# Kernel optimization log

Measured on AMD Instinct MI355X. Metric: run time of the kernel, lower is better.

The kernel has to match this reference:

```python
import jax, jax.numpy as jnp
import numpy as np

G = 16       # groups
GRID = 25    # hardcoded self.grid
EPS = 1e-5   # BatchNorm eps


def _gconv(x, w, pad):
    # x: (B, Cin, H, W), w: (Cout, Cin//G, kh, kw); grouped conv, stride 1
    return jax.lax.conv_general_dilated(
        x, w, window_strides=(1, 1), padding=[(pad, pad), (pad, pad)],
        feature_group_count=G)


def _bn_relu(h, g, b, m, v):
    # h: (G, B, C, H, W); per-group-instance BN params: (G, C). Inference BN.
    scale = (g / jnp.sqrt(v + EPS))[:, None, :, None, None]
    return jax.nn.relu((h - m[:, None, :, None, None]) * scale + b[:, None, :, None, None])


def setup_inputs() -> dict:
    key = jax.random.key(0)
    ks = jax.random.split(key, 11)
    B, C, H, W = 2, 256, 24, 24
    AC = GRID * C  # 6400 affinity channels
    return {
        "x":  jax.random.normal(ks[0], (B, C, H, W), jnp.float32),
        "W1": jax.random.normal(ks[1], (G, C, C // G, 3, 3), jnp.float32) * 0.05,
        "g1": jax.random.uniform(ks[2], (G, C), jnp.float32, 0.5, 1.5),
        "b1": jax.random.normal(ks[3], (G, C), jnp.float32) * 0.1,
        "m1": jax.random.normal(ks[4], (G, C), jnp.float32) * 0.1,
        "v1": jax.random.uniform(ks[5], (G, C), jnp.float32, 0.5, 1.5),
        "W2": jax.random.normal(ks[6], (G, AC, C // G, 1, 1), jnp.float32) * 0.05,
        "g2": jax.random.uniform(ks[7], (G, AC), jnp.float32, 0.5, 1.5),
        "b2": jax.random.normal(ks[8], (G, AC), jnp.float32) * 0.1,
        "m2": jax.random.normal(ks[9], (G, AC), jnp.float32) * 0.1,
        "v2": jax.random.uniform(ks[10], (G, AC), jnp.float32, 0.5, 1.5),
    }


def reference(x, W1, g1, b1, m1, v1, W2, g2, b2, m2, v2):
    B, C, H, W = x.shape
    Cg = C // G
    # 16 independent grouped 3x3 convs over the same input, batched via vmap
    h1 = jax.vmap(lambda w: _gconv(x, w, 1))(W1)          # (G, B, C, H, W)
    h1 = _bn_relu(h1, g1, b1, m1, v1)
    # grouped 1x1 conv with padding=1 (faithful to source -> spatial grows to H+2, W+2)
    a = jax.vmap(lambda h, w: _gconv(h, w, 1))(h1, W2)    # (G, B, 25C, H+2, W+2)
    a = _bn_relu(a, g2, b2, m2, v2)
    pooled = a.mean(axis=(-2, -1))                        # adaptive avg pool -> (G, B, 25C)
    xv = pooled.reshape(G, B, G, GRID * Cg)               # (G, B, G, 25*Cg)
    aff = jnp.einsum('ibkm,iblm->ibkl', xv, xv)           # (G, B, G, G) = theta @ phi
    idx = jnp.arange(G)
    aff_i = aff[idx, :, idx, :] / G                       # aff[:, i], /N  -> (G, B, G)
    ex = h1.reshape(G, B, G, Cg * H * W)
    # torch.matmul((B,G), (B,G,M)) broadcasts 2-D lhs -> (B, B, M); kept faithfully
    z = jnp.einsum('ipk,iqkm->ipqm', aff_i, ex)           # (G, B, B, Cg*H*W)
    z = z.reshape(G, B, B, Cg, H, W).transpose(1, 0, 2, 3, 4, 5)
    return z.reshape(B, G * B * Cg, H, W)                 # (B, B*C, H, W)
```

## Files before the change

kernel.cpp:

```cpp
#include <hip/hip_runtime.h>
#include <hip/hip_bf16.h>


typedef __attribute__((ext_vector_type(8))) short short8;
typedef __attribute__((ext_vector_type(4))) short short4v;
typedef __attribute__((ext_vector_type(4))) float f32x4;

static __device__ __forceinline__ short f2bf(float x) {
    unsigned u = __float_as_uint(x);
    unsigned r = (u + 0x7fffu + ((u >> 16) & 1u)) >> 16;
    return (short)r;
}

__global__ __launch_bounds__(256) void k1_conv_mfma(
    const float* __restrict__ xin,
    const float* __restrict__ W1,
    const float* __restrict__ g1, const float* __restrict__ b1,
    const float* __restrict__ m1, const float* __restrict__ v1,
    float* __restrict__ h1f)
{
    __shared__ __align__(16) short xs[27*26*24];
    __shared__ __align__(16) short wA[5*16*40];
    __shared__ float scale_s[16], bias_s[16];

    int bid = blockIdx.x;
    int i = bid >> 5, b = (bid >> 4) & 1, g = bid & 15;
    int t = threadIdx.x;

    int* xz = (int*)xs;
    for (int idx = t; idx < 27*26*12; idx += 256) xz[idx] = 0;
    if (t < 16) {
        int c = i*256 + g*16 + t;
        float sc = g1[c] * rsqrtf(v1[c] + 1e-5f);
        scale_s[t] = sc;
        bias_s[t]  = b1[c] - m1[c] * sc;
    }
    __syncthreads();

    const float* xb = &xin[(b*256 + g*16)*576];
    for (int idx = t; idx < 9216; idx += 256) {
        int ci = idx / 576; int s = idx - ci*576;
        int y = s / 24; int x = s - y*24;
        xs[((y+1)*26 + (x+1))*24 + ci] = f2bf(xb[idx]);
    }
    const float* wb = &W1[(i*256 + g*16)*144];
    for (int idx = t; idx < 2560; idx += 256) {
        int kk = idx >> 9, rem = idx & 511, co = rem >> 5, k = rem & 31;
        int tap = 2*kk + (k >> 4), ci = k & 15;
        float val = (tap < 9) ? wb[co*144 + ci*9 + tap] * scale_s[co] : 0.f;
        wA[(kk*16 + co)*40 + k] = f2bf(val);
    }
    __syncthreads();

    int l = t & 63, w = t >> 6;
    int quad = l >> 4, col = l & 15;
    int ci0 = (quad & 1) * 8;

    short8 afr[5];
#pragma unroll
    for (int kk = 0; kk < 5; kk++)
        afr[kk] = *(const short8*)&wA[(kk*16 + col)*40 + quad*8];

    f32x4 cb = *(const f32x4*)&bias_s[quad*4];

    const int offE[5] = {0, 48, 648, 1248, 1296};
    const int offO[5] = {24, 624, 672, 1272, 1872};
    int off[5];
#pragma unroll
    for (int kk = 0; kk < 5; kk++) off[kk] = (quad >= 2) ? offO[kk] : offE[kk];

    float* hout = &h1f[((i*2 + b)*256 + g*16)*576];
#pragma unroll 3
    for (int tt = 0; tt < 9; tt++) {
        int tile = w*9 + tt;
        int s = tile*16 + col;
        int y = s / 24; int x = s - y*24;
        int base = (y*26 + x)*24 + ci0;
        f32x4 acc = cb;
#pragma unroll
        for (int kk = 0; kk < 5; kk++) {
            short8 bf = *(const short8*)&xs[base + off[kk]];
            acc = __builtin_amdgcn_mfma_f32_16x16x32_bf16(afr[kk], bf, acc, 0, 0, 0);
        }
#pragma unroll
        for (int r = 0; r < 4; r++)
            hout[(quad*4 + r)*576 + s] = fmaxf(acc[r], 0.f);
    }
}

__global__ __launch_bounds__(256) void k2_pool_mfma(
    const float* __restrict__ h1f,
    const float* __restrict__ W2,
    const float* __restrict__ g2, const float* __restrict__ b2,
    const float* __restrict__ m2, const float* __restrict__ v2,
    float* __restrict__ pooled)
{
    __shared__ __align__(16) short hsb[576*20];
    __shared__ __align__(16) short wlb[400*16];
    __shared__ __align__(16) float psum[4*400];
    __shared__ __align__(16) float bias_s[400];

    int bid = blockIdx.x;
    int i = bid >> 5, b = (bid >> 4) & 1, k = bid & 15;
    int t = threadIdx.x;

    const float* hbase = &h1f[((i*2 + b)*256 + k*16)*576];
    for (int idx = t; idx < 9216; idx += 256) {
        int j = idx / 576; int s = idx - j*576;
        hsb[s*20 + j] = f2bf(hbase[idx]);
    }
    for (int m = t; m < 400; m += 256) {
        int o = i*6400 + k*400 + m;
        float s2 = g2[o] * rsqrtf(v2[o] + 1e-5f);
        bias_s[m] = b2[o] - m2[o] * s2;
        const float4* wr = (const float4*)&W2[o*16];
#pragma unroll
        for (int q = 0; q < 4; q++) {
            float4 wv = wr[q];
            wlb[m*16 + q*4 + 0] = f2bf(wv.x * s2);
            wlb[m*16 + q*4 + 1] = f2bf(wv.y * s2);
            wlb[m*16 + q*4 + 2] = f2bf(wv.z * s2);
            wlb[m*16 + q*4 + 3] = f2bf(wv.w * s2);
        }
    }
    __syncthreads();

    int l = t & 63, w = t >> 6;
    int half = l >> 4;
    int col  = l & 15;

    short8 bfr[9];
#pragma unroll
    for (int u = 0; u < 9; u++) {
        if (l < 32) {
            const short* p = &hsb[((w*9 + u)*16 + col)*20 + half*8];
            short4v lo = *(const short4v*)p;
            short4v hi = *(const short4v*)(p + 4);
            short8 f; f[0]=lo.x; f[1]=lo.y; f[2]=lo.z; f[3]=lo.w;
                      f[4]=hi.x; f[5]=hi.y; f[6]=hi.z; f[7]=hi.w;
            bfr[u] = f;
        } else {
            bfr[u] = (short8)0;
        }
    }

    for (int mt = 0; mt < 25; mt++) {
        short8 af = (short8)0;
        if (l < 32)
            af = *(const short8*)&wlb[(mt*16 + col)*16 + half*8];

        f32x4 cb = *(const f32x4*)&bias_s[mt*16 + half*4];

        f32x4 d[9];
#pragma unroll
        for (int u = 0; u < 9; u++)
            d[u] = __builtin_amdgcn_mfma_f32_16x16x32_bf16(af, bfr[u], cb, 0, 0, 0);

        float p0=0.f, p1=0.f, p2=0.f, p3=0.f;
#pragma unroll
        for (int u = 0; u < 9; u++) {
            p0 += fmaxf(d[u][0], 0.f);
            p1 += fmaxf(d[u][1], 0.f);
            p2 += fmaxf(d[u][2], 0.f);
            p3 += fmaxf(d[u][3], 0.f);
        }
#pragma unroll
        for (int msk = 1; msk < 16; msk <<= 1) {
            p0 += __shfl_xor(p0, msk);
            p1 += __shfl_xor(p1, msk);
            p2 += __shfl_xor(p2, msk);
            p3 += __shfl_xor(p3, msk);
        }
        if (col == 0) {
            f32x4 pv = {p0, p1, p2, p3};
            *(f32x4*)&psum[w*400 + mt*16 + half*4] = pv;
        }
    }
    __syncthreads();

    const float inv = 1.f / 676.f;
    for (int m = t; m < 400; m += 256) {
        float s = psum[0*400+m] + psum[1*400+m] + psum[2*400+m] + psum[3*400+m];
        float be = bias_s[m];
        pooled[(i*2+b)*6400 + k*400 + m] = (s + 100.f * fmaxf(be, 0.f)) * inv;
    }
}

__global__ __launch_bounds__(256) void k3_aff(const float* __restrict__ pooled,
                                              float* __restrict__ aff)
{
    __shared__ float th[400];
    __shared__ float parts[256];
    int bid = blockIdx.x;
    int i = bid >> 1;
    int t = threadIdx.x;
    const float* pb = &pooled[bid*6400];
    for (int idx = t; idx < 400; idx += 256) th[idx] = pb[i*400 + idx];
    __syncthreads();
    int l = t >> 4, p = t & 15;
    float sum = 0.f;
    const float* pl = &pb[l*400];
    for (int m = p*25; m < p*25 + 25; m++) sum = fmaf(th[m], pl[m], sum);
    parts[t] = sum;
    __syncthreads();
    if (t < 16) {
        float s = 0.f;
        for (int pp = 0; pp < 16; pp++) s += parts[t*16 + pp];
        aff[bid*16 + t] = s * (1.f/16.f);
    }
}

__global__ __launch_bounds__(256) void k4_out(const float* __restrict__ h1f,
                                              const float* __restrict__ aff,
                                              float* __restrict__ out)
{
    __shared__ float a0[16], a1[16];
    int bid = blockIdx.x;
    int i = bid >> 5, q = (bid >> 4) & 1, cg = bid & 15;
    int t = threadIdx.x;
    if (t < 16) a0[t] = aff[(i*2+0)*16 + t];
    else if (t < 32) a1[t-16] = aff[(i*2+1)*16 + (t-16)];
    __syncthreads();
    const float* hb = &h1f[((i*2+q)*256 + cg)*576];
    int ch = i*32 + q*16 + cg;
    for (int s = t; s < 576; s += 256) {
        float acc0 = 0.f, acc1 = 0.f;
#pragma unroll
        for (int k = 0; k < 16; k++) {
            float v = hb[k*9216 + s];
            acc0 = fmaf(a0[k], v, acc0);
            acc1 = fmaf(a1[k], v, acc1);
        }
        out[ch*576 + s]         = acc0;
        out[(512 + ch)*576 + s] = acc1;
    }
}

extern "C" void kernel_launch(void* const* d_in, const int* in_sizes, int n_in,
                              void* d_out, int out_size, void* d_ws, size_t ws_size,
                              hipStream_t stream)
{
    const float* x  = (const float*)d_in[0];
    const float* W1 = (const float*)d_in[1];
    const float* g1 = (const float*)d_in[2];
    const float* b1 = (const float*)d_in[3];
    const float* m1 = (const float*)d_in[4];
    const float* v1 = (const float*)d_in[5];
    const float* W2 = (const float*)d_in[6];
    const float* g2 = (const float*)d_in[7];
    const float* b2 = (const float*)d_in[8];
    const float* m2 = (const float*)d_in[9];
    const float* v2 = (const float*)d_in[10];

    float* h1f    = (float*)d_ws;
    float* pooled = h1f + 16*2*256*576;
    float* aff    = pooled + 16*2*6400;

    float* out = (float*)d_out;

    hipLaunchKernelGGL(k1_conv_mfma, dim3(512), dim3(256), 0, stream,
                       x, W1, g1, b1, m1, v1, h1f);
    hipLaunchKernelGGL(k2_pool_mfma, dim3(512), dim3(256), 0, stream,
                       h1f, W2, g2, b2, m2, v2, pooled);
    hipLaunchKernelGGL(k3_aff,       dim3(32),  dim3(256), 0, stream,
                       pooled, aff);
    hipLaunchKernelGGL(k4_out,       dim3(512), dim3(256), 0, stream,
                       h1f, aff, out);
}
```

Measured before the change: 126.5 us.

## Fuse grouped 3x3 conv and 1x1-conv pooling kernels via shared LDS

Merges the conv+BN+ReLU kernel and the 1x1 conv+BN+ReLU+pool kernel into one block-per-(i,b,g) kernel. The conv output stays in registers, is packed to bf16 straight into a reused LDS region, and feeds the second MFMA stage without a global round trip. h1f is still written to global because the final kernel reads it. This removes one launch and the global reread and conversion of h1f, at the cost of a larger fused kernel with more register pressure (9 accumulators held across a barrier).

Result: slower. 129.2 us (+2.1%).

```diff
diff --git a/kernel.cpp b/kernel.cpp
--- a/kernel.cpp
+++ b/kernel.cpp
@@ -12,16 +12,25 @@
     return (short)r;
 }
 
-__global__ __launch_bounds__(256) void k1_conv_mfma(
+__global__ __launch_bounds__(256) void k12_fused(
     const float* __restrict__ xin,
     const float* __restrict__ W1,
     const float* __restrict__ g1, const float* __restrict__ b1,
     const float* __restrict__ m1, const float* __restrict__ v1,
-    float* __restrict__ h1f)
-{
-    __shared__ __align__(16) short xs[27*26*24];
-    __shared__ __align__(16) short wA[5*16*40];
-    __shared__ float scale_s[16], bias_s[16];
+    const float* __restrict__ W2,
+    const float* __restrict__ g2, const float* __restrict__ b2,
+    const float* __restrict__ m2, const float* __restrict__ v2,
+    float* __restrict__ h1f,
+    float* __restrict__ pooled)
+{
+    __shared__ __align__(16) char smem[43840];
+    short* xs    = (short*)smem;
+    short* wA    = (short*)(smem + 33696);
+    short* hsb   = (short*)smem;
+    short* wlb   = (short*)(smem + 23040);
+    float* psum  = (float*)(smem + 35840);
+    float* bias2 = (float*)(smem + 42240);
+    __shared__ float scale1[16], bias1[16];
 
     int bid = blockIdx.x;
     int i = bid >> 5, b = (bid >> 4) & 1, g = bid & 15;
@@ -32,8 +41,8 @@
     if (t < 16) {
         int c = i*256 + g*16 + t;
         float sc = g1[c] * rsqrtf(v1[c] + 1e-5f);
-        scale_s[t] = sc;
-        bias_s[t]  = b1[c] - m1[c] * sc;
+        scale1[t] = sc;
+        bias1[t]  = b1[c] - m1[c] * sc;
     }
     __syncthreads();
 
@@ -47,72 +56,66 @@
     for (int idx = t; idx < 2560; idx += 256) {
         int kk = idx >> 9, rem = idx & 511, co = rem >> 5, k = rem & 31;
         int tap = 2*kk + (k >> 4), ci = k & 15;
-        float val = (tap < 9) ? wb[co*144 + ci*9 + tap] * scale_s[co] : 0.f;
+        float val = (tap < 9) ? wb[co*144 + ci*9 + tap] * scale1[co] : 0.f;
         wA[(kk*16 + co)*40 + k] = f2bf(val);
     }
     __syncthreads();
 
     int l = t & 63, w = t >> 6;
     int quad = l >> 4, col = l & 15;
-    int ci0 = (quad & 1) * 8;
-
-    short8 afr[5];
-#pragma unroll
-    for (int kk = 0; kk < 5; kk++)
-        afr[kk] = *(const short8*)&wA[(kk*16 + col)*40 + quad*8];
-
-    f32x4 cb = *(const f32x4*)&bias_s[quad*4];
-
-    const int offE[5] = {0, 48, 648, 1248, 1296};
-    const int offO[5] = {24, 624, 672, 1272, 1872};
-    int off[5];
-#pragma unroll
-    for (int kk = 0; kk < 5; kk++) off[kk] = (quad >= 2) ? offO[kk] : offE[kk];
-
-    float* hout = &h1f[((i*2 + b)*256 + g*16)*576];
+    {
+        int ci0 = (quad & 1) * 8;
+        short8 afr[5];
+#pragma unroll
+        for (int kk = 0; kk < 5; kk++)
+            afr[kk] = *(const short8*)&wA[(kk*16 + col)*40 + quad*8];
+        f32x4 cb1 = *(const f32x4*)&bias1[quad*4];
+
+        const int offE[5] = {0, 48, 648, 1248, 1296};
+        const int offO[5] = {24, 624, 672, 1272, 1872};
+        int off[5];
+#pragma unroll
+        for (int kk = 0; kk < 5; kk++) off[kk] = (quad >= 2) ? offO[kk] : offE[kk];
+
+        f32x4 dreg[9];
 #pragma unroll 3
-    for (int tt = 0; tt < 9; tt++) {
-        int tile = w*9 + tt;
-        int s = tile*16 + col;
-        int y = s / 24; int x = s - y*24;
-        int base = (y*26 + x)*24 + ci0;
-        f32x4 acc = cb;
-#pragma unroll
-        for (int kk = 0; kk < 5; kk++) {
-            short8 bf = *(const short8*)&xs[base + off[kk]];
-            acc = __builtin_amdgcn_mfma_f32_16x16x32_bf16(afr[kk], bf, acc, 0, 0, 0);
-        }
-#pragma unroll
-        for (int r = 0; r < 4; r++)
-            hout[(quad*4 + r)*576 + s] = fmaxf(acc[r], 0.f);
-    }
-}
-
-__global__ __launch_bounds__(256) void k2_pool_mfma(
-    const float* __restrict__ h1f,
-    const float* __restrict__ W2,
-    const float* __restrict__ g2, const float* __restrict__ b2,
-    const float* __restrict__ m2, const float* __restrict__ v2,
-    float* __restrict__ pooled)
-{
-    __shared__ __align__(16) short hsb[576*20];
-    __shared__ __align__(16) short wlb[400*16];
-    __shared__ __align__(16) float psum[4*400];
-    __shared__ __align__(16) float bias_s[400];
-
-    int bid = blockIdx.x;
-    int i = bid >> 5, b = (bid >> 4) & 1, k = bid & 15;
-    int t = threadIdx.x;
-
-    const float* hbase = &h1f[((i*2 + b)*256 + k*16)*576];
-    for (int idx = t; idx < 9216; idx += 256) {
-        int j = idx / 576; int s = idx - j*576;
-        hsb[s*20 + j] = f2bf(hbase[idx]);
-    }
+        for (int tt = 0; tt < 9; tt++) {
+            int s = (w*9 + tt)*16 + col;
+            int y = s / 24; int x = s - y*24;
+            int base = (y*26 + x)*24 + ci0;
+            f32x4 acc = cb1;
+#pragma unroll
+            for (int kk = 0; kk < 5; kk++) {
+                short8 bf = *(const short8*)&xs[base + off[kk]];
+                acc = __builtin_amdgcn_mfma_f32_16x16x32_bf16(afr[kk], bf, acc, 0, 0, 0);
+            }
+#pragma unroll
+            for (int r = 0; r < 4; r++) acc[r] = fmaxf(acc[r], 0.f);
+            dreg[tt] = acc;
+        }
+        __syncthreads();
+
+        float* hout = &h1f[((i*2 + b)*256 + g*16)*576];
+#pragma unroll
+        for (int tt = 0; tt < 9; tt++) {
+            int s = (w*9 + tt)*16 + col;
+            f32x4 acc = dreg[tt];
+            unsigned p0 = (unsigned)(unsigned short)f2bf(acc[0]) |
+                          ((unsigned)(unsigned short)f2bf(acc[1]) << 16);
+            unsigned p1 = (unsigned)(unsigned short)f2bf(acc[2]) |
+                          ((unsigned)(unsigned short)f2bf(acc[3]) << 16);
+            uint2 pk = {p0, p1};
+            *(uint2*)&hsb[s*20 + quad*4] = pk;
+#pragma unroll
+            for (int r = 0; r < 4; r++)
+                hout[(quad*4 + r)*576 + s] = acc[r];
+        }
+    }
+
     for (int m = t; m < 400; m += 256) {
-        int o = i*6400 + k*400 + m;
+        int o = i*6400 + g*400 + m;
         float s2 = g2[o] * rsqrtf(v2[o] + 1e-5f);
-        bias_s[m] = b2[o] - m2[o] * s2;
+        bias2[m] = b2[o] - m2[o] * s2;
         const float4* wr = (const float4*)&W2[o*16];
 #pragma unroll
         for (int q = 0; q < 4; q++) {
@@ -125,55 +128,54 @@
     }
     __syncthreads();
 
-    int l = t & 63, w = t >> 6;
     int half = l >> 4;
-    int col  = l & 15;
-
-    short8 bfr[9];
-#pragma unroll
-    for (int u = 0; u < 9; u++) {
-        if (l < 32) {
-            const short* p = &hsb[((w*9 + u)*16 + col)*20 + half*8];
-            short4v lo = *(const short4v*)p;
-            short4v hi = *(const short4v*)(p + 4);
-            short8 f; f[0]=lo.x; f[1]=lo.y; f[2]=lo.z; f[3]=lo.w;
-                      f[4]=hi.x; f[5]=hi.y; f[6]=hi.z; f[7]=hi.w;
-            bfr[u] = f;
-        } else {
-            bfr[u] = (short8)0;
-        }
-    }
-
-    for (int mt = 0; mt < 25; mt++) {
-        short8 af = (short8)0;
-        if (l < 32)
-            af = *(const short8*)&wlb[(mt*16 + col)*16 + half*8];
-
-        f32x4 cb = *(const f32x4*)&bias_s[mt*16 + half*4];
-
-        f32x4 d[9];
-#pragma unroll
-        for (int u = 0; u < 9; u++)
-            d[u] = __builtin_amdgcn_mfma_f32_16x16x32_bf16(af, bfr[u], cb, 0, 0, 0);
-
-        float p0=0.f, p1=0.f, p2=0.f, p3=0.f;
+    {
+        short8 bfr[9];
 #pragma unroll
         for (int u = 0; u < 9; u++) {
-            p0 += fmaxf(d[u][0], 0.f);
-            p1 += fmaxf(d[u][1], 0.f);
-            p2 += fmaxf(d[u][2], 0.f);
-            p3 += fmaxf(d[u][3], 0.f);
-        }
-#pragma unroll
-        for (int msk = 1; msk < 16; msk <<= 1) {
-            p0 += __shfl_xor(p0, msk);
-            p1 += __shfl_xor(p1, msk);
-            p2 += __shfl_xor(p2, msk);
-            p3 += __shfl_xor(p3, msk);
-        }
-        if (col == 0) {
-            f32x4 pv = {p0, p1, p2, p3};
-            *(f32x4*)&psum[w*400 + mt*16 + half*4] = pv;
+            if (l < 32) {
+                const short* p = &hsb[((w*9 + u)*16 + col)*20 + half*8];
+                short4v lo = *(const short4v*)p;
+                short4v hi = *(const short4v*)(p + 4);
+                short8 f; f[0]=lo.x; f[1]=lo.y; f[2]=lo.z; f[3]=lo.w;
+                          f[4]=hi.x; f[5]=hi.y; f[6]=hi.z; f[7]=hi.w;
+                bfr[u] = f;
+            } else {
+                bfr[u] = (short8)0;
+            }
+        }
+
+        for (int mt = 0; mt < 25; mt++) {
+            short8 af = (short8)0;
+            if (l < 32)
+                af = *(const short8*)&wlb[(mt*16 + col)*16 + half*8];
+
+            f32x4 cb = *(const f32x4*)&bias2[mt*16 + half*4];
+
+            f32x4 d[9];
+#pragma unroll
+            for (int u = 0; u < 9; u++)
+                d[u] = __builtin_amdgcn_mfma_f32_16x16x32_bf16(af, bfr[u], cb, 0, 0, 0);
+
+            float p0=0.f, p1=0.f, p2=0.f, p3=0.f;
+#pragma unroll
+            for (int u = 0; u < 9; u++) {
+                p0 += fmaxf(d[u][0], 0.f);
+                p1 += fmaxf(d[u][1], 0.f);
+                p2 += fmaxf(d[u][2], 0.f);
+                p3 += fmaxf(d[u][3], 0.f);
+            }
+#pragma unroll
+            for (int msk = 1; msk < 16; msk <<= 1) {
+                p0 += __shfl_xor(p0, msk);
+                p1 += __shfl_xor(p1, msk);
+                p2 += __shfl_xor(p2, msk);
+                p3 += __shfl_xor(p3, msk);
+            }
+            if (col == 0) {
+                f32x4 pv = {p0, p1, p2, p3};
+                *(f32x4*)&psum[w*400 + mt*16 + half*4] = pv;
+            }
         }
     }
     __syncthreads();
@@ -181,8 +183,8 @@
     const float inv = 1.f / 676.f;
     for (int m = t; m < 400; m += 256) {
         float s = psum[0*400+m] + psum[1*400+m] + psum[2*400+m] + psum[3*400+m];
-        float be = bias_s[m];
-        pooled[(i*2+b)*6400 + k*400 + m] = (s + 100.f * fmaxf(be, 0.f)) * inv;
+        float be = bias2[m];
+        pooled[(i*2+b)*6400 + g*400 + m] = (s + 100.f * fmaxf(be, 0.f)) * inv;
     }
 }
 
@@ -258,12 +260,10 @@
 
     float* out = (float*)d_out;
 
-    hipLaunchKernelGGL(k1_conv_mfma, dim3(512), dim3(256), 0, stream,
-                       x, W1, g1, b1, m1, v1, h1f);
-    hipLaunchKernelGGL(k2_pool_mfma, dim3(512), dim3(256), 0, stream,
-                       h1f, W2, g2, b2, m2, v2, pooled);
-    hipLaunchKernelGGL(k3_aff,       dim3(32),  dim3(256), 0, stream,
+    hipLaunchKernelGGL(k12_fused, dim3(512), dim3(256), 0, stream,
+                       x, W1, g1, b1, m1, v1, W2, g2, b2, m2, v2, h1f, pooled);
+    hipLaunchKernelGGL(k3_aff,    dim3(32),  dim3(256), 0, stream,
                        pooled, aff);
-    hipLaunchKernelGGL(k4_out,       dim3(512), dim3(256), 0, stream,
+    hipLaunchKernelGGL(k4_out,    dim3(512), dim3(256), 0, stream,
                        h1f, aff, out);
 }
```
